# Kernel tuning notes

Measured on AMD Instinct MI355X. Metric: run time of the kernel, lower is better.

Reference implementation:

```python
import jax, jax.numpy as jnp
import numpy as np

DIM = 768
NUM_HEADS = 12
HEAD_DIM = DIM // NUM_HEADS  # 64


def setup_inputs() -> dict:
    key = jax.random.key(0)
    k1, k2, k3, k4 = jax.random.split(key, 4)
    B, N = 2, 2048
    x = jax.random.normal(k1, (B, N, DIM), dtype=jnp.float32)
    att_mask = jnp.ones((B, N), dtype=jnp.int32)
    # learned params (qkv has no bias since qkv_bias=False)
    qkv_w = jax.random.normal(k2, (3 * DIM, DIM), dtype=jnp.float32) * (1.0 / np.sqrt(DIM))
    proj_w = jax.random.normal(k3, (DIM, DIM), dtype=jnp.float32) * (1.0 / np.sqrt(DIM))
    proj_b = jax.random.normal(k4, (DIM,), dtype=jnp.float32) * 0.02
    return {"x": x, "att_mask": att_mask, "qkv_w": qkv_w, "proj_w": proj_w, "proj_b": proj_b}


def reference(x, att_mask, qkv_w, proj_w, proj_b):
    B, N, C = x.shape
    H, Dh = NUM_HEADS, HEAD_DIM
    scale = Dh ** (-0.5)
    # qkv projection: [B,N,3C] -> [3,B,H,N,Dh]
    qkv = jnp.einsum('bnc,oc->bno', x, qkv_w)
    qkv = qkv.reshape(B, N, 3, H, Dh).transpose(2, 0, 3, 1, 4)
    q, k, v = qkv[0], qkv[1], qkv[2]
    q = q * scale
    # full N x N logits (the memory-bound hotspot)
    logit = jnp.einsum('bhnd,bhmd->bhnm', q, k)
    # 2D mask path: [B,N] -> [B,1,1,N], masked_fill(mask==0, -inf)
    mask = att_mask[:, None, None, :]
    logit = jnp.where(mask == 0, -jnp.inf, logit)
    attn = jax.nn.softmax(logit, axis=-1)  # attn_drop is identity (p=0, eval)
    out = jnp.einsum('bhnm,bhmd->bhnd', attn, v)
    out = out.transpose(0, 2, 1, 3).reshape(B, N, H * Dh)
    out = jnp.einsum('bnc,oc->bno', out, proj_w) + proj_b  # proj_drop identity
    return out
```

## Files before the change

### kernel.cpp

```cpp
#include <hip/hip_runtime.h>
#include <hip/hip_bf16.h>
#include <math.h>
#include <cstdint>
#include <cstddef>

typedef __bf16 bf16x8 __attribute__((ext_vector_type(8)));
typedef __bf16 bf16x4 __attribute__((ext_vector_type(4)));
typedef short  s16x4  __attribute__((ext_vector_type(4)));
typedef float  f32x4  __attribute__((ext_vector_type(4)));

#define GLOAD16(g, l) __builtin_amdgcn_global_load_lds( \
    (const __attribute__((address_space(1))) void*)(g),  \
    (__attribute__((address_space(3))) void*)(l), 16, 0, 0)

__device__ __forceinline__ unsigned short f2bf(float f) {
    union { float f; unsigned u; } v; v.f = f;
    unsigned u = v.u;
    u += 0x7fffu + ((u >> 16) & 1u);
    return (unsigned short)(u >> 16);
}

__device__ __forceinline__ unsigned pack_bf16x2(float a, float b) {
    __hip_bfloat162 h = __float22bfloat162_rn(make_float2(a, b));
    return *reinterpret_cast<unsigned*>(&h);
}

__device__ __forceinline__ f32x4 mfma16(bf16x4 a, bf16x4 b, f32x4 c) {
#if __has_builtin(__builtin_amdgcn_mfma_f32_16x16x16_bf16)
    return __builtin_amdgcn_mfma_f32_16x16x16_bf16(a, b, c, 0, 0, 0);
#elif __has_builtin(__builtin_amdgcn_mfma_f32_16x16x16bf16_1k)
    return __builtin_amdgcn_mfma_f32_16x16x16bf16_1k(
        __builtin_bit_cast(s16x4, a), __builtin_bit_cast(s16x4, b), c, 0, 0, 0);
#else
    asm volatile("v_mfma_f32_16x16x16_bf16 %0, %1, %2, %0"
                 : "+v"(c) : "v"(a), "v"(b));
    return c;
#endif
}

__global__ __launch_bounds__(256) void cvt_all(
    const float* __restrict__ x,
    const float* __restrict__ qkvw,
    const float* __restrict__ projw,
    unsigned short* __restrict__ xb,
    unsigned short* __restrict__ wqkv,
    unsigned short* __restrict__ wproj)
{
    const int N1 = 4096 * 768;
    const int N2 = 2304 * 768;
    const int SC = 768 * 768;
    const float C2 = 0.18033688011112042f;
    int i = ((int)blockIdx.x * 256 + (int)threadIdx.x) * 4;

    const float* src;
    unsigned short* dst;
    int j;
    bool sc = false;
    if (i < N1)           { src = x;     dst = xb;    j = i; }
    else if (i < N1 + N2) { j = i - N1;  src = qkvw;  dst = wqkv;  sc = (j < SC); }
    else                  { j = i - N1 - N2; src = projw; dst = wproj; }

    float4 v = *reinterpret_cast<const float4*>(src + j);
    if (sc) { v.x *= C2; v.y *= C2; v.z *= C2; v.w *= C2; }
    uint2 pk;
    pk.x = pack_bf16x2(v.x, v.y);
    pk.y = pack_bf16x2(v.z, v.w);
    *reinterpret_cast<uint2*>(dst + j) = pk;
}

template <int MODE, int MROWS, int NF>
__global__ __launch_bounds__(256) void gemm_bt(
    const unsigned short* __restrict__ A,
    const unsigned short* __restrict__ B,
    unsigned short* __restrict__ Cb,
    unsigned short* __restrict__ Vt,
    float* __restrict__ Cf,
    const float* __restrict__ bias,
    int M, int N, int K)
{
    constexpr int MI = MROWS / 32;
    __shared__ __align__(16) unsigned short Al[2][MROWS * 64];
    __shared__ __align__(16) unsigned short Bl[2][NF * 32 * 64];
    const int bm   = blockIdx.x * MROWS;
    const int bn   = blockIdx.y * (NF * 32);
    const int tid  = (int)threadIdx.x;
    const int wave = tid >> 6;
    const int lane = tid & 63;
    const int wr   = wave >> 1;
    const int wc   = wave & 1;
    const int q    = lane & 15;
    const int g4   = (lane >> 4) * 4;

    f32x4 acc[MI][NF] = {};

    const int srow = lane >> 3;
    const int scol = (lane & 7) * 8;

    auto stage = [&](int buf, int k0) {
#pragma unroll
        for (int i = 0; i < MI; ++i) {
            const int chunk = wave * MI + i;
            GLOAD16(A + (size_t)(bm + chunk * 8 + srow) * K + (k0 + scol),
                    &Al[buf][chunk * 512]);
        }
#pragma unroll
        for (int i = 0; i < NF; ++i) {
            const int chunk = wave * NF + i;
            GLOAD16(B + (size_t)(bn + chunk * 8 + srow) * K + (k0 + scol),
                    &Bl[buf][chunk * 512]);
        }
    };

    stage(0, 0);
    __syncthreads();

    const int nt = K / 64;
    int buf = 0;
    for (int t = 0; t < nt; ++t) {
        if (t + 1 < nt) stage(buf ^ 1, (t + 1) * 64);
#pragma unroll
        for (int kk = 0; kk < 2; ++kk) {
            const int ko = kk * 32 + (lane >> 4) * 8;
            bf16x8 af[MI], bf[NF];
#pragma unroll
            for (int mi = 0; mi < MI; ++mi)
                af[mi] = *(const bf16x8*)&Al[buf][(wr * (MROWS / 2) + mi * 16 + q) * 64 + ko];
#pragma unroll
            for (int ni = 0; ni < NF; ++ni)
                bf[ni] = *(const bf16x8*)&Bl[buf][(wc * 16 * NF + ni * 16 + q) * 64 + ko];
#pragma unroll
            for (int mi = 0; mi < MI; ++mi)
#pragma unroll
                for (int ni = 0; ni < NF; ++ni)
                    acc[mi][ni] = __builtin_amdgcn_mfma_f32_16x16x32_bf16(
                        af[mi], bf[ni], acc[mi][ni], 0, 0, 0);
        }
        __syncthreads();
        buf ^= 1;
    }

#pragma unroll
    for (int mi = 0; mi < MI; ++mi) {
        const int row0 = bm + wr * (MROWS / 2) + mi * 16 + g4;
        if constexpr (MODE == 1) {
#pragma unroll
            for (int ni = 0; ni < NF; ++ni) {
                const int col = bn + wc * 16 * NF + ni * 16 + q;
#pragma unroll
                for (int r = 0; r < 4; ++r)
                    Cf[(size_t)(row0 + r) * N + col] = acc[mi][ni][r] + bias[col];
            }
        } else {
            if (bn < 1536) {
#pragma unroll
                for (int ni = 0; ni < NF; ++ni) {
                    const int col = bn + wc * 16 * NF + ni * 16 + q;
#pragma unroll
                    for (int r = 0; r < 4; ++r)
                        Cb[(size_t)(row0 + r) * 1536 + col] = f2bf(acc[mi][ni][r]);
                }
            } else {
                const int bb  = row0 >> 11;
                const int np  = row0 & 2047;
                const int tt  = np >> 6;
                const int wv  = (np >> 4) & 3;
                const int gg  = (np >> 2) & 3;
#pragma unroll
                for (int ni = 0; ni < NF; ++ni) {
                    const int vcol = bn + wc * 16 * NF + ni * 16 + q - 1536;
                    const int hv = vcol >> 6, d = vcol & 63;
                    const size_t idx =
                        ((size_t)((bb * 12 + hv) * 32 + tt) * 4 + wv) * 1024
                        + gg * 256 + d * 4;
                    uint2 w;
                    w.x = pack_bf16x2(acc[mi][ni][0], acc[mi][ni][1]);
                    w.y = pack_bf16x2(acc[mi][ni][2], acc[mi][ni][3]);
                    *reinterpret_cast<uint2*>(&Vt[idx]) = w;
                }
            }
        }
    }
}

__global__ __launch_bounds__(256, 3) void attn_fwd(
    const unsigned short* __restrict__ qk,
    const unsigned short* __restrict__ vT,
    const int* __restrict__ mask,
    unsigned short* __restrict__ out)
{
    const int NN = 2048, H = 12;
    const int bid = (int)blockIdx.x;
    const int bhh = (bid & 7) * 3 + ((bid >> 3) >> 5);
    const int qt  = (bid >> 3) & 31;
    const int b   = bhh / H, h = bhh % H;
    const int q0  = qt * 64;
    const int tid = (int)threadIdx.x, wave = tid >> 6, lane = tid & 63;
    const int g   = lane >> 4;
    const int q   = lane & 15;
    const int swz = (q & 7) << 3;

    __shared__ __align__(16) unsigned short LDS[16896];
    unsigned short* Kl0 = LDS;
    unsigned short* Vl0 = LDS + 8192;

    bool allone;
    {
        const int* mrow = mask + b * NN + lane * 32;
        unsigned mv = 0xFFFFFFFFu;
#pragma unroll
        for (int i = 0; i < 8; ++i) {
            int4 m = *reinterpret_cast<const int4*>(mrow + i * 4);
            mv = min(mv, min(min((unsigned)m.x, (unsigned)m.y),
                             min((unsigned)m.z, (unsigned)m.w)));
        }
        allone = __all(mv != 0u);
    }

    bf16x8 qf[2][4];
#pragma unroll
    for (int kk = 0; kk < 2; ++kk)
#pragma unroll
        for (int qtl = 0; qtl < 4; ++qtl)
            qf[kk][qtl] = *reinterpret_cast<const bf16x8*>(
                &qk[(size_t)(b * NN + q0 + 16 * qtl + q) * 1536 + h * 64 + kk * 32 + g * 8]);

    const char* kg0 = (const char*)(qk + (size_t)(b * NN + wave * 16 + (lane >> 3)) * 1536
                                    + 768 + h * 64 + ((lane & 7) ^ (lane >> 3)) * 8);
    const char* kg1 = kg0 + (size_t)8 * 1536 * 2;
    const unsigned short* vgp = vT + ((size_t)bhh * 32 * 4 + wave) * 1024 + lane * 8;

    auto stageK = [&](int buf) {
        GLOAD16(kg0, &Kl0[buf * 4096 + wave * 1024]);
        GLOAD16(kg1, &Kl0[buf * 4096 + wave * 1024 + 512]);
        kg0 += (size_t)64 * 1536 * 2;
        kg1 += (size_t)64 * 1536 * 2;
    };
    auto stageV = [&](int buf) {
        GLOAD16(vgp,       &Vl0[buf * 4096 + wave * 1024]);
        GLOAD16(vgp + 512, &Vl0[buf * 4096 + wave * 1024 + 512]);
        vgp += 4096;
    };

    f32x4 oacc[4][4] = {};
    float l[4] = {0.f, 0.f, 0.f, 0.f};

    stageK(0); stageV(0);

    int cur = 0;
    for (int it = 0; it < 32; ++it) {
        if (it < 31) { stageK(cur ^ 1); stageV(cur ^ 1); }

        if (it < 31) asm volatile("s_waitcnt vmcnt(6)" ::: "memory");
        else         asm volatile("s_waitcnt vmcnt(2)" ::: "memory");

        f32x4 s[4] = {};
        __builtin_amdgcn_s_setprio(1);
#pragma unroll
        for (int kk = 0; kk < 2; ++kk) {
            bf16x8 kf = *(const bf16x8*)&Kl0[cur * 4096 + (16 * wave + q) * 64
                                             + ((kk * 32 + g * 8) ^ swz)];
#pragma unroll
            for (int qtl = 0; qtl < 4; ++qtl)
                s[qtl] = __builtin_amdgcn_mfma_f32_16x16x32_bf16(kf, qf[kk][qtl], s[qtl], 0, 0, 0);
        }
        __builtin_amdgcn_s_setprio(0);

        if (!allone) {
            int4 mr = *reinterpret_cast<const int4*>(
                &mask[b * NN + it * 64 + 16 * wave + 4 * g]);
#pragma unroll
            for (int qtl = 0; qtl < 4; ++qtl) {
                if (mr.x == 0) s[qtl][0] = -INFINITY;
                if (mr.y == 0) s[qtl][1] = -INFINITY;
                if (mr.z == 0) s[qtl][2] = -INFINITY;
                if (mr.w == 0) s[qtl][3] = -INFINITY;
            }
        }

        bf16x4 pb[4];
#pragma unroll
        for (int qtl = 0; qtl < 4; ++qtl) {
            float p0 = __builtin_amdgcn_exp2f(s[qtl][0]);
            float p1 = __builtin_amdgcn_exp2f(s[qtl][1]);
            float p2 = __builtin_amdgcn_exp2f(s[qtl][2]);
            float p3 = __builtin_amdgcn_exp2f(s[qtl][3]);
            l[qtl] += (p0 + p1) + (p2 + p3);
            uint2 t;
            t.x = pack_bf16x2(p0, p1);
            t.y = pack_bf16x2(p2, p3);
            pb[qtl] = __builtin_bit_cast(bf16x4, t);
        }

        if (it < 31) asm volatile("s_waitcnt vmcnt(4)" ::: "memory");
        else         asm volatile("s_waitcnt vmcnt(0)" ::: "memory");

        __builtin_amdgcn_s_setprio(1);
#pragma unroll
        for (int ct = 0; ct < 4; ++ct) {
            bf16x4 va = *(const bf16x4*)&Vl0[cur * 4096 + wave * 1024
                                             + g * 256 + (16 * ct + q) * 4];
#pragma unroll
            for (int qtl = 0; qtl < 4; ++qtl)
                oacc[ct][qtl] = mfma16(va, pb[qtl], oacc[ct][qtl]);
        }
        __builtin_amdgcn_s_setprio(0);

        cur ^= 1;
    }

    __syncthreads();

#pragma unroll
    for (int qtl = 0; qtl < 4; ++qtl) {
        l[qtl] += __shfl_xor(l[qtl], 16);
        l[qtl] += __shfl_xor(l[qtl], 32);
    }
    float* lb = (float*)&LDS[16384];
    float* fb = (float*)&LDS[0];
    if (g == 0) {
#pragma unroll
        for (int qtl = 0; qtl < 4; ++qtl) lb[wave * 64 + qtl * 16 + q] = l[qtl];
    }
    if (wave & 1) {
        float* dst = fb + (wave >> 1) * 4096;
#pragma unroll
        for (int ct = 0; ct < 4; ++ct)
#pragma unroll
            for (int qtl = 0; qtl < 4; ++qtl)
                *reinterpret_cast<f32x4*>(&dst[(ct * 4 + qtl) * 256 + lane * 4]) = oacc[ct][qtl];
    }
    __syncthreads();
    if (!(wave & 1)) {
        float* srcp = fb + (wave >> 1) * 4096;
#pragma unroll
        for (int ct = 0; ct < 4; ++ct)
#pragma unroll
            for (int qtl = 0; qtl < 4; ++qtl)
                oacc[ct][qtl] += *reinterpret_cast<f32x4*>(&srcp[(ct * 4 + qtl) * 256 + lane * 4]);
    }
    __syncthreads();
    if (wave == 2) {
#pragma unroll
        for (int ct = 0; ct < 4; ++ct)
#pragma unroll
            for (int qtl = 0; qtl < 4; ++qtl)
                *reinterpret_cast<f32x4*>(&fb[(ct * 4 + qtl) * 256 + lane * 4]) = oacc[ct][qtl];
    }
    __syncthreads();
    if (wave == 0) {
        float inv[4];
#pragma unroll
        for (int qtl = 0; qtl < 4; ++qtl)
            inv[qtl] = 1.0f / (lb[qtl * 16 + q] + lb[64 + qtl * 16 + q]
                              + lb[128 + qtl * 16 + q] + lb[192 + qtl * 16 + q]);
#pragma unroll
        for (int ct = 0; ct < 4; ++ct)
#pragma unroll
            for (int qtl = 0; qtl < 4; ++qtl) {
                f32x4 o = oacc[ct][qtl]
                        + *reinterpret_cast<f32x4*>(&fb[(ct * 4 + qtl) * 256 + lane * 4]);
                uint2 ow;
                ow.x = pack_bf16x2(o[0] * inv[qtl], o[1] * inv[qtl]);
                ow.y = pack_bf16x2(o[2] * inv[qtl], o[3] * inv[qtl]);
                *reinterpret_cast<uint2*>(
                    &out[(size_t)(b * NN + q0 + 16 * qtl + q) * 768 + h * 64 + 16 * ct + 4 * g]) = ow;
            }
    }
}

extern "C" void kernel_launch(void* const* d_in, const int* in_sizes, int n_in,
                              void* d_out, int out_size, void* d_ws, size_t ws_size,
                              hipStream_t stream)
{
    const float* x      = (const float*)d_in[0];
    const int*   mask   = (const int*)d_in[1];
    const float* qkv_w  = (const float*)d_in[2];
    const float* proj_w = (const float*)d_in[3];
    const float* proj_b = (const float*)d_in[4];
    float* out = (float*)d_out;

    const int BN = 2 * 2048;
    const int C  = 768;
    const int C3 = 2304;

    char* w = (char*)d_ws;
    unsigned short* xb    = (unsigned short*)w; w += (size_t)BN * C    * 2;
    unsigned short* wqkv  = (unsigned short*)w; w += (size_t)C3 * C    * 2;
    unsigned short* wproj = (unsigned short*)w; w += (size_t)C  * C    * 2;
    unsigned short* qk    = (unsigned short*)w; w += (size_t)BN * 1536 * 2;
    unsigned short* vT    = (unsigned short*)w; w += (size_t)24 * 64 * 2048 * 2;
    unsigned short* ao    = (unsigned short*)w;

    {
        const int total = (BN * C + C3 * C + C * C) / 4;
        cvt_all<<<total / 256, 256, 0, stream>>>(x, qkv_w, proj_w, xb, wqkv, wproj);
    }

    gemm_bt<2, 128, 4><<<dim3(BN / 128, C3 / 128), 256, 0, stream>>>(
        xb, wqkv, qk, vT, nullptr, nullptr, BN, C3, C);

    attn_fwd<<<dim3(768), 256, 0, stream>>>(qk, vT, mask, ao);

    gemm_bt<1, 64, 2><<<dim3(BN / 64, C / 64), 256, 0, stream>>>(
        ao, wproj, nullptr, nullptr, out, proj_b, BN, C, C);
}
```

Baseline: 105.1 us.

## Software-pipeline QK^T one tile ahead with triple-buffered V and swizzle GEMM LDS

The attention loop is restructured so the QK^T MFMAs for the next key tile are issued before the PV MFMAs of the current tile, using two score register sets and a triple-buffered V staging area in enlarged LDS. This is meant to overlap softmax exp work and memory waits with matrix work across iterations. Separately, the projection GEMM's LDS tiles now use an XOR column swizzle on both the staging writes and the fragment reads to reduce bank conflicts. The cost is more registers and LDS per block, which may lower occupancy, plus more complex waitcnt bookkeeping.

Result: no change. 103.8 us (-1.2%).

```diff
diff --git a/kernel.cpp b/kernel.cpp
--- a/kernel.cpp
+++ b/kernel.cpp
@@ -90,11 +90,12 @@
     const int wc   = wave & 1;
     const int q    = lane & 15;
     const int g4   = (lane >> 4) * 4;
+    const int swz  = (q & 7) << 3;
 
     f32x4 acc[MI][NF] = {};
 
     const int srow = lane >> 3;
-    const int scol = (lane & 7) * 8;
+    const int scol = ((lane & 7) ^ srow) * 8;
 
     auto stage = [&](int buf, int k0) {
 #pragma unroll
@@ -124,10 +125,12 @@
             bf16x8 af[MI], bf[NF];
 #pragma unroll
             for (int mi = 0; mi < MI; ++mi)
-                af[mi] = *(const bf16x8*)&Al[buf][(wr * (MROWS / 2) + mi * 16 + q) * 64 + ko];
+                af[mi] = *(const bf16x8*)&Al[buf][(wr * (MROWS / 2) + mi * 16 + q) * 64
+                                                  + (ko ^ swz)];
 #pragma unroll
             for (int ni = 0; ni < NF; ++ni)
-                bf[ni] = *(const bf16x8*)&Bl[buf][(wc * 16 * NF + ni * 16 + q) * 64 + ko];
+                bf[ni] = *(const bf16x8*)&Bl[buf][(wc * 16 * NF + ni * 16 + q) * 64
+                                                  + (ko ^ swz)];
 #pragma unroll
             for (int mi = 0; mi < MI; ++mi)
 #pragma unroll
@@ -199,7 +202,7 @@
     const int q   = lane & 15;
     const int swz = (q & 7) << 3;
 
-    __shared__ __align__(16) unsigned short LDS[16896];
+    __shared__ __align__(16) unsigned short LDS[20480];
     unsigned short* Kl0 = LDS;
     unsigned short* Vl0 = LDS + 8192;
 
@@ -243,69 +246,85 @@
 
     f32x4 oacc[4][4] = {};
     float l[4] = {0.f, 0.f, 0.f, 0.f};
-
-    stageK(0); stageV(0);
-
-    int cur = 0;
-    for (int it = 0; it < 32; ++it) {
-        if (it < 31) { stageK(cur ^ 1); stageV(cur ^ 1); }
-
-        if (it < 31) asm volatile("s_waitcnt vmcnt(6)" ::: "memory");
-        else         asm volatile("s_waitcnt vmcnt(2)" ::: "memory");
-
-        f32x4 s[4] = {};
+    f32x4 sA[4], sB[4];
+
+    auto qkstep = [&](f32x4* sdst, int kb) {
         __builtin_amdgcn_s_setprio(1);
 #pragma unroll
         for (int kk = 0; kk < 2; ++kk) {
-            bf16x8 kf = *(const bf16x8*)&Kl0[cur * 4096 + (16 * wave + q) * 64
+            bf16x8 kf = *(const bf16x8*)&Kl0[kb * 4096 + (16 * wave + q) * 64
                                              + ((kk * 32 + g * 8) ^ swz)];
 #pragma unroll
             for (int qtl = 0; qtl < 4; ++qtl)
-                s[qtl] = __builtin_amdgcn_mfma_f32_16x16x32_bf16(kf, qf[kk][qtl], s[qtl], 0, 0, 0);
+                sdst[qtl] = __builtin_amdgcn_mfma_f32_16x16x32_bf16(
+                    kf, qf[kk][qtl], sdst[qtl], 0, 0, 0);
         }
         __builtin_amdgcn_s_setprio(0);
-
+    };
+
+    stageK(0); stageV(0); stageK(1); stageV(1);
+    asm volatile("s_waitcnt vmcnt(6)" ::: "memory");
+#pragma unroll
+    for (int qtl = 0; qtl < 4; ++qtl) sA[qtl] = f32x4{0.f, 0.f, 0.f, 0.f};
+    qkstep(sA, 0);
+
+    int vcur = 0, vstg = 2;
+    bf16x4 pb[4];
+
+    auto body = [&](f32x4* scur, f32x4* snxt, int t) {
         if (!allone) {
             int4 mr = *reinterpret_cast<const int4*>(
-                &mask[b * NN + it * 64 + 16 * wave + 4 * g]);
+                &mask[b * NN + t * 64 + 16 * wave + 4 * g]);
 #pragma unroll
             for (int qtl = 0; qtl < 4; ++qtl) {
-                if (mr.x == 0) s[qtl][0] = -INFINITY;
-                if (mr.y == 0) s[qtl][1] = -INFINITY;
-                if (mr.z == 0) s[qtl][2] = -INFINITY;
-                if (mr.w == 0) s[qtl][3] = -INFINITY;
+                if (mr.x == 0) scur[qtl][0] = -INFINITY;
+                if (mr.y == 0) scur[qtl][1] = -INFINITY;
+                if (mr.z == 0) scur[qtl][2] = -INFINITY;
+                if (mr.w == 0) scur[qtl][3] = -INFINITY;
             }
         }
-
-        bf16x4 pb[4];
 #pragma unroll
         for (int qtl = 0; qtl < 4; ++qtl) {
-            float p0 = __builtin_amdgcn_exp2f(s[qtl][0]);
-            float p1 = __builtin_amdgcn_exp2f(s[qtl][1]);
-            float p2 = __builtin_amdgcn_exp2f(s[qtl][2]);
-            float p3 = __builtin_amdgcn_exp2f(s[qtl][3]);
+            float p0 = __builtin_amdgcn_exp2f(scur[qtl][0]);
+            float p1 = __builtin_amdgcn_exp2f(scur[qtl][1]);
+            float p2 = __builtin_amdgcn_exp2f(scur[qtl][2]);
+            float p3 = __builtin_amdgcn_exp2f(scur[qtl][3]);
             l[qtl] += (p0 + p1) + (p2 + p3);
-            uint2 t;
-            t.x = pack_bf16x2(p0, p1);
-            t.y = pack_bf16x2(p2, p3);
-            pb[qtl] = __builtin_bit_cast(bf16x4, t);
-        }
-
-        if (it < 31) asm volatile("s_waitcnt vmcnt(4)" ::: "memory");
-        else         asm volatile("s_waitcnt vmcnt(0)" ::: "memory");
+            uint2 tt;
+            tt.x = pack_bf16x2(p0, p1);
+            tt.y = pack_bf16x2(p2, p3);
+            pb[qtl] = __builtin_bit_cast(bf16x4, tt);
+        }
+
+        if (t <= 29) { stageK(t & 1); stageV(vstg); }
+        vstg = (vstg == 2) ? 0 : vstg + 1;
+
+        if (t <= 29)      asm volatile("s_waitcnt vmcnt(6)" ::: "memory");
+        else if (t == 30) asm volatile("s_waitcnt vmcnt(2)" ::: "memory");
+        else              asm volatile("s_waitcnt vmcnt(0)" ::: "memory");
+
+        if (t <= 30) {
+#pragma unroll
+            for (int qtl = 0; qtl < 4; ++qtl) snxt[qtl] = f32x4{0.f, 0.f, 0.f, 0.f};
+            qkstep(snxt, (t + 1) & 1);
+        }
 
         __builtin_amdgcn_s_setprio(1);
 #pragma unroll
         for (int ct = 0; ct < 4; ++ct) {
-            bf16x4 va = *(const bf16x4*)&Vl0[cur * 4096 + wave * 1024
+            bf16x4 va = *(const bf16x4*)&Vl0[vcur * 4096 + wave * 1024
                                              + g * 256 + (16 * ct + q) * 4];
 #pragma unroll
             for (int qtl = 0; qtl < 4; ++qtl)
                 oacc[ct][qtl] = mfma16(va, pb[qtl], oacc[ct][qtl]);
         }
         __builtin_amdgcn_s_setprio(0);
-
-        cur ^= 1;
+        vcur = (vcur == 2) ? 0 : vcur + 1;
+    };
+
+    for (int tt = 0; tt < 16; ++tt) {
+        body(sA, sB, 2 * tt);
+        body(sB, sA, 2 * tt + 1);
     }
 
     __syncthreads();
```

## Triple-buffer GEMM K-loop with 32-wide tiles and XOR-swizzled LDS layout

Applied to the files above, without the earlier changes.

Replaces the double-buffered 64-wide K staging in the projection GEMM with a three-stage ring of 32-wide K tiles. Raw s_waitcnt vmcnt plus s_barrier lets two tiles of global-to-LDS loads stay in flight while the current tile is computed, and drops the trailing __syncthreads. An XOR swizzle on the LDS column index is applied to both the async stores and the fragment reads to reduce bank conflicts. The risks are a hand-counted vmcnt that must match the number of outstanding loads per stage, and less MFMA work per barrier.

Measured after the change: 91.77 us, median of 2. -12.7%, faster.

```diff
diff --git a/kernel.cpp b/kernel.cpp
--- a/kernel.cpp
+++ b/kernel.cpp
@@ -79,8 +79,11 @@
     int M, int N, int K)
 {
     constexpr int MI = MROWS / 32;
-    __shared__ __align__(16) unsigned short Al[2][MROWS * 64];
-    __shared__ __align__(16) unsigned short Bl[2][NF * 32 * 64];
+    constexpr int AC = MROWS / 64;
+    constexpr int BC = NF / 2;
+    constexpr int NL = AC + BC;
+    __shared__ __align__(16) unsigned short Al[3][MROWS * 32];
+    __shared__ __align__(16) unsigned short Bl[3][NF * 32 * 32];
     const int bm   = blockIdx.x * MROWS;
     const int bn   = blockIdx.y * (NF * 32);
     const int tid  = (int)threadIdx.x;
@@ -89,54 +92,59 @@
     const int wr   = wave >> 1;
     const int wc   = wave & 1;
     const int q    = lane & 15;
-    const int g4   = (lane >> 4) * 4;
+    const int g    = lane >> 4;
+    const int g4   = g * 4;
+    const int rswz = (g ^ ((q >> 1) & 3)) << 3;
 
     f32x4 acc[MI][NF] = {};
 
-    const int srow = lane >> 3;
-    const int scol = (lane & 7) * 8;
+    const int srow = lane >> 2;
+    const int scol = ((lane & 3) ^ ((lane >> 3) & 3)) << 3;
 
     auto stage = [&](int buf, int k0) {
 #pragma unroll
-        for (int i = 0; i < MI; ++i) {
-            const int chunk = wave * MI + i;
-            GLOAD16(A + (size_t)(bm + chunk * 8 + srow) * K + (k0 + scol),
+        for (int i = 0; i < AC; ++i) {
+            const int chunk = wave * AC + i;
+            GLOAD16(A + (size_t)(bm + chunk * 16 + srow) * K + (k0 + scol),
                     &Al[buf][chunk * 512]);
         }
 #pragma unroll
-        for (int i = 0; i < NF; ++i) {
-            const int chunk = wave * NF + i;
-            GLOAD16(B + (size_t)(bn + chunk * 8 + srow) * K + (k0 + scol),
+        for (int i = 0; i < BC; ++i) {
+            const int chunk = wave * BC + i;
+            GLOAD16(B + (size_t)(bn + chunk * 16 + srow) * K + (k0 + scol),
                     &Bl[buf][chunk * 512]);
         }
     };
 
     stage(0, 0);
-    __syncthreads();
-
-    const int nt = K / 64;
-    int buf = 0;
+    stage(1, 32);
+
+    const int nt = K / 32;
     for (int t = 0; t < nt; ++t) {
-        if (t + 1 < nt) stage(buf ^ 1, (t + 1) * 64);
-#pragma unroll
-        for (int kk = 0; kk < 2; ++kk) {
-            const int ko = kk * 32 + (lane >> 4) * 8;
-            bf16x8 af[MI], bf[NF];
-#pragma unroll
-            for (int mi = 0; mi < MI; ++mi)
-                af[mi] = *(const bf16x8*)&Al[buf][(wr * (MROWS / 2) + mi * 16 + q) * 64 + ko];
+        const int cur = t % 3;
+        if (t < nt - 1) {
+            if constexpr (NL == 4)
+                asm volatile("s_waitcnt vmcnt(4)\n\ts_barrier" ::: "memory");
+            else
+                asm volatile("s_waitcnt vmcnt(2)\n\ts_barrier" ::: "memory");
+        } else {
+            asm volatile("s_waitcnt vmcnt(0)\n\ts_barrier" ::: "memory");
+        }
+        if (t + 2 < nt) stage((cur + 2) % 3, (t + 2) * 32);
+
+        bf16x8 af[MI], bf[NF];
+#pragma unroll
+        for (int mi = 0; mi < MI; ++mi)
+            af[mi] = *(const bf16x8*)&Al[cur][(wr * (MROWS / 2) + mi * 16 + q) * 32 + rswz];
+#pragma unroll
+        for (int ni = 0; ni < NF; ++ni)
+            bf[ni] = *(const bf16x8*)&Bl[cur][(wc * 16 * NF + ni * 16 + q) * 32 + rswz];
+#pragma unroll
+        for (int mi = 0; mi < MI; ++mi)
 #pragma unroll
             for (int ni = 0; ni < NF; ++ni)
-                bf[ni] = *(const bf16x8*)&Bl[buf][(wc * 16 * NF + ni * 16 + q) * 64 + ko];
-#pragma unroll
-            for (int mi = 0; mi < MI; ++mi)
-#pragma unroll
-                for (int ni = 0; ni < NF; ++ni)
-                    acc[mi][ni] = __builtin_amdgcn_mfma_f32_16x16x32_bf16(
-                        af[mi], bf[ni], acc[mi][ni], 0, 0, 0);
-        }
-        __syncthreads();
-        buf ^= 1;
+                acc[mi][ni] = __builtin_amdgcn_mfma_f32_16x16x32_bf16(
+                    af[mi], bf[ni], acc[mi][ni], 0, 0, 0);
     }
 
 #pragma unroll
```
